# Kernel tuning notes

Hardware: AMD Instinct MI355X
Metric: run time of the kernel (lower is better)

## Reference

```python
import jax, jax.numpy as jnp
import numpy as np

NDIM = 128
GDIM = 128
NUM_LAYERS = 2
B = 8192
IDX = 16          # nodes per graph
EPG = 32          # edges per graph
N = B * IDX       # total nodes = 131072
E = B * EPG       # total edges = 262144


def setup_inputs() -> dict:
    key = jax.random.key(0)
    ks = jax.random.split(key, 24)
    h = jax.random.normal(ks[0], (B, IDX, NDIM), dtype=jnp.float32)
    # edges constrained within each graph (flattened node indexing)
    gid = jnp.repeat(jnp.arange(B, dtype=jnp.int64), EPG)
    src = gid * IDX + jax.random.randint(ks[1], (E,), 0, IDX).astype(jnp.int64)
    dst = gid * IDX + jax.random.randint(ks[2], (E,), 0, IDX).astype(jnp.int64)
    edge_index = jnp.stack([src, dst], axis=0)
    s = 0.05
    inp = {
        'h': h,
        'edge_index': edge_index,
        'msg_W': jax.random.normal(ks[3], (NUM_LAYERS, 2 * NDIM, 2 * NDIM), jnp.float32) * s,
        'msg_b': jax.random.normal(ks[4], (NUM_LAYERS, 2 * NDIM), jnp.float32) * s,
        'msgr_W': jax.random.normal(ks[5], (NUM_LAYERS, 2 * NDIM, 2 * NDIM), jnp.float32) * s,
        'msgr_b': jax.random.normal(ks[6], (NUM_LAYERS, 2 * NDIM), jnp.float32) * s,
        'gru_Wih': jax.random.normal(ks[7], (NUM_LAYERS, 3 * NDIM, 2 * NDIM), jnp.float32) * s,
        'gru_Whh': jax.random.normal(ks[8], (NUM_LAYERS, 3 * NDIM, NDIM), jnp.float32) * s,
        'gru_bih': jax.random.normal(ks[9], (NUM_LAYERS, 3 * NDIM), jnp.float32) * s,
        'gru_bhh': jax.random.normal(ks[10], (NUM_LAYERS, 3 * NDIM), jnp.float32) * s,
        'fm_W': jax.random.normal(ks[11], (GDIM, NDIM), jnp.float32) * s,
        'fm_b': jax.random.normal(ks[12], (GDIM,), jnp.float32) * s,
        'gm_W': jax.random.normal(ks[13], (1, NDIM), jnp.float32) * s,
        'gm_b': jax.random.normal(ks[14], (1,), jnp.float32) * s,
        'fmi_W': jax.random.normal(ks[15], (GDIM, NDIM), jnp.float32) * s,
        'fmi_b': jax.random.normal(ks[16], (GDIM,), jnp.float32) * s,
        'gmi_W': jax.random.normal(ks[17], (1, NDIM), jnp.float32) * s,
        'gmi_b': jax.random.normal(ks[18], (1,), jnp.float32) * s,
    }
    return inp


def _gnn_forward(h, edge_index, msg_W, msg_b, msgr_W, msgr_b,
                 gru_Wih, gru_Whh, gru_bih, gru_bhh):
    # h: [N, ndim]; edge_index: [2, E] -> doubled with reversed edges -> [2, 2E]
    ei = jnp.concatenate([edge_index, edge_index[::-1]], axis=1)
    src, dst = ei[0], ei[1]
    e = edge_index.shape[1]
    n_nodes = h.shape[0]
    for l in range(NUM_LAYERS):
        # (eval mode: dropout p=0.0 is a no-op)
        h_j = h[src]                       # [2E, ndim]
        h_i = h[dst]                       # [2E, ndim]
        m = jnp.concatenate([h_j, h_i], axis=1)   # [2E, 2*ndim]
        m_fwd, m_rev = m[:e], m[e:]
        a = jnp.concatenate([
            m_fwd @ msg_W[l].T + msg_b[l],
            m_rev @ msgr_W[l].T + msgr_b[l],
        ], axis=0)                          # [2E, 2*ndim]
        aggr = jax.ops.segment_sum(a, dst, num_segments=n_nodes)  # [N, 2*ndim]
        # GRUCell(aggr, h): gate order r, z, n (torch convention)
        gi = aggr @ gru_Wih[l].T + gru_bih[l]   # [N, 3*ndim]
        gh = h @ gru_Whh[l].T + gru_bhh[l]      # [N, 3*ndim]
        gi_r, gi_z, gi_n = jnp.split(gi, 3, axis=1)
        gh_r, gh_z, gh_n = jnp.split(gh, 3, axis=1)
        r = jax.nn.sigmoid(gi_r + gh_r)
        z = jax.nn.sigmoid(gi_z + gh_z)
        n = jnp.tanh(gi_n + r * gh_n)
        h = n + z * (h - n)                 # (1-z)*n + z*h
    return h


def _graph_aggr(h, idx, f_W, f_b, g_W, g_b):
    # gated sum aggregation
    h_vG = h @ f_W.T + f_b                      # [N, gdim]
    g_vG = jax.nn.sigmoid(h @ g_W.T + g_b)      # [N, 1]
    out = (h_vG * g_vG).reshape(-1, idx, f_W.shape[0])
    return out.sum(axis=1)                      # [B, gdim]


def reference(h, edge_index, msg_W, msg_b, msgr_W, msgr_b,
              gru_Wih, gru_Whh, gru_bih, gru_bhh,
              fm_W, fm_b, gm_W, gm_b, fmi_W, fmi_b, gmi_W, gmi_b):
    idx = h.shape[1]
    hf = h.reshape(-1, NDIM)
    hf = _gnn_forward(hf, edge_index, msg_W, msg_b, msgr_W, msgr_b,
                      gru_Wih, gru_Whh, gru_bih, gru_bhh)
    h_G = _graph_aggr(hf, idx, fm_W, fm_b, gm_W, gm_b)
    h_G_init = _graph_aggr(hf, idx, fmi_W, fmi_b, gmi_W, gmi_b)
    return (hf.reshape(-1, idx, NDIM), h_G, h_G_init)
```

## Files before the change

### kernel.cpp

```cpp
#include <hip/hip_runtime.h>
#include <math.h>
#include <stdint.h>

#define NDIM 128
#define B_GRAPHS 8192
#define IDX 16
#define EPG 32
#define NN (B_GRAPHS*IDX)
#define NE (B_GRAPHS*EPG)

typedef short bf16x8 __attribute__((ext_vector_type(8)));
typedef float f32x4  __attribute__((ext_vector_type(4)));

__device__ inline unsigned short f2bf(float x) {
    union { float f; unsigned u; } v; v.f = x;
    unsigned r = v.u + 0x7fff + ((v.u >> 16) & 1);
    return (unsigned short)(r >> 16);
}
__device__ inline float bf2f(unsigned short b) {
    union { unsigned u; float f; } v; v.u = ((unsigned)b) << 16;
    return v.f;
}
__device__ inline float sigm(float x) { return 1.f/(1.f + __expf(-x)); }
__device__ inline float tanh_f(float x) {
    float ax = fabsf(x);
    float t  = __expf(-2.f*ax);
    float r  = (1.f - t)/(1.f + t);
    return copysignf(r, x);
}

#define GLOAD_LDS16(g, l) \
    __builtin_amdgcn_global_load_lds( \
        (const __attribute__((address_space(1))) unsigned int*)(g), \
        (__attribute__((address_space(3))) unsigned int*)(l), 16, 0, 0)

__global__ __launch_bounds__(256) void compose_kernel(
    const float* __restrict__ msg_W, const float* __restrict__ msgr_W,
    const float* __restrict__ Wih,   const float* __restrict__ Whh,
    const float* __restrict__ msg_b, const float* __restrict__ msgr_b,
    unsigned short* __restrict__ WB, float* __restrict__ c34)
{
    int idx = blockIdx.x*256 + threadIdx.x;
    const int TWB = 2*512*640;
    if (idx < TWB) {
        int l = idx / (512*640); int rem = idx - l*(512*640);
        int cold = rem / 640; int k = rem - cold*640;
        float val;
        if (k < 512) {
            if (cold < 384) {
                const float* wih = Wih + l*384*256 + cold*256;
                const float* M; int sc;
                if (k < 128)      { M = msg_W  + l*256*256; sc = k;       }
                else if (k < 256) { M = msgr_W + l*256*256; sc = k - 128; }
                else if (k < 384) { M = msg_W  + l*256*256; sc = k - 128; }
                else              { M = msgr_W + l*256*256; sc = k - 256; }
                float acc = 0.f;
                for (int q = 0; q < 256; q++) acc = fmaf(wih[q], M[q*256 + sc], acc);
                val = acc;
            } else val = 0.f;
        } else {
            int kk = k - 512;
            if (cold < 256)      val = Whh[l*384*128 + cold*128 + kk];
            else if (cold < 384) val = 0.f;
            else                 val = Whh[l*384*128 + (cold-128)*128 + kk];
        }
        int cc = cold & 127, t = cold >> 7;
        int colp = ((cc >> 4) << 6) + (t << 4) + (cc & 15);
        WB[l*512*640 + colp*640 + k] = f2bf(val);
    } else if (idx < TWB + 2*2*384) {
        int i2 = idx - TWB;
        int l = i2 / 768; int rem = i2 - l*768;
        int which = rem / 384; int r = rem - which*384;
        const float* wih = Wih + l*384*256 + r*256;
        const float* bb  = (which ? msgr_b : msg_b) + l*256;
        float acc = 0.f;
        for (int q = 0; q < 256; q++) acc = fmaf(wih[q], bb[q], acc);
        c34[l*768 + which*384 + r] = acc;
    }
}

__global__ __launch_bounds__(128) void init_kernel(
    const float* __restrict__ hin, const int* __restrict__ ei,
    unsigned short* __restrict__ A, float* __restrict__ indeg,
    float* __restrict__ outdeg, unsigned char* __restrict__ pack)
{
    int g = blockIdx.x, t = threadIdx.x;
    __shared__ float hb[16][128];
    __shared__ float sin_[16][128];
    __shared__ float sout_[16][128];
    __shared__ int sl[32], dl[32];
    __shared__ int cin[16], cout[16];
    __shared__ int flag64;
    int base = g*IDX;
    for (int r = 0; r < 16; r++) hb[r][t] = hin[(size_t)(base+r)*128 + t];
    for (int r = 0; r < 16; r++) { sin_[r][t] = 0.f; sout_[r][t] = 0.f; }
    if (t < 16) { cin[t] = 0; cout[t] = 0; }
    if (t == 0) {
        int orv = 0;
        for (int i = 1; i < 64; i += 2) orv |= ei[i];
        flag64 = (orv == 0);
    }
    __syncthreads();
    if (t < 32) {
        int e = g*EPG + t;
        int sv, dv;
        if (flag64) { sv = ei[2*e]; dv = ei[2*(NE + e)]; }
        else        { sv = ei[e];   dv = ei[NE + e];     }
        sl[t] = sv - base; dl[t] = dv - base;
        atomicAdd(&cout[sl[t]], 1); atomicAdd(&cin[dl[t]], 1);
        pack[g*32 + t] = (unsigned char)((sl[t] & 15) | ((dl[t] & 15) << 4));
    }
    __syncthreads();
    for (int e = 0; e < 32; e++) {
        sin_[dl[e]][t]  += hb[sl[e]][t];
        sout_[sl[e]][t] += hb[dl[e]][t];
    }
    for (int r = 0; r < 16; r++) {
        size_t v = base + r;
        float di = (float)cin[r], dof = (float)cout[r];
        A[v*640 + t]        = f2bf(sin_[r][t]);
        A[v*640 + 128 + t]  = f2bf(sout_[r][t]);
        A[v*640 + 256 + t]  = f2bf(di  * hb[r][t]);
        A[v*640 + 384 + t]  = f2bf(dof * hb[r][t]);
        A[v*640 + 512 + t]  = f2bf(hb[r][t]);
    }
    if (t < 16) { indeg[base+t] = (float)cin[t]; outdeg[base+t] = (float)cout[t]; }
}

struct FSmem {
    unsigned short As[3][128*32];
    union {
        unsigned short Bs[3][384*32];
        unsigned short hnewB[128*128];
    } u;
    unsigned char csr[8][2][17];
    unsigned char adj[8][2][32];
    unsigned char offj[8][2][16];
    float gates[2][128];
};

__device__ __forceinline__ int h_addr(int row, int c) {
    return row*256 + (((c>>3) ^ (row&7))<<4) + ((c&7)<<1);
}

#define MF(a,b,c) __builtin_amdgcn_mfma_f32_16x16x32_bf16((a),(b),(c),0,0,0)

#define CSTEP(BUF, J2) do {                                                   \
    const unsigned short* Asb = sm.As[BUF];                                   \
    const unsigned short* Bsb = sm.u.Bs[BUF];                                 \
    bf16x8 bfv[3];                                                            \
    _Pragma("unroll")                                                         \
    for (int t = 0; t < 3; t++) {                                             \
        int a0 = wid*48 + t*16 + l15;                                         \
        bfv[t] = *(const bf16x8*)(Bsb + a0*32 + (l4 ^ ((a0>>2)&3))*8);        \
    }                                                                         \
    _Pragma("unroll")                                                         \
    for (int mi = 0; mi < 8; mi++) {                                          \
        int row = mi*16 + l15;                                                \
        bf16x8 af = *(const bf16x8*)(Asb + row*32 + (l4 ^ ((row>>2)&3))*8);   \
        acc[mi][0]  = MF(af, bfv[0], acc[mi][0]);                             \
        acc[mi][1]  = MF(af, bfv[1], acc[mi][1]);                             \
        acc[mi][J2] = MF(af, bfv[2], acc[mi][J2]);                            \
    }                                                                         \
} while (0)

template <bool FINAL>
__global__ __launch_bounds__(512, 2) void fused_kernel(
    unsigned short* __restrict__ A,
    const unsigned short* __restrict__ WBl,
    const float* __restrict__ indeg, const float* __restrict__ outdeg,
    const unsigned char* __restrict__ pack,
    const float* __restrict__ c34l,
    const float* __restrict__ bihl, const float* __restrict__ bhhl,
    const float* __restrict__ gmW,  const float* __restrict__ gmb,
    const float* __restrict__ gmiW, const float* __restrict__ gmib,
    float* __restrict__ hf, float* __restrict__ P1, float* __restrict__ P2,
    float* __restrict__ sg)
{
    __shared__ FSmem sm;
    const int n0  = blockIdx.x * 128;
    const int g0  = blockIdx.x * 8;
    const int tid = threadIdx.x;
    const int lane = tid & 63, wid = tid >> 6;
    const int l15 = lane & 15, l4 = lane >> 4;

    const int arow = tid >> 2, as_ = tid & 3;
    const int asrc = (as_ ^ ((arow >> 2) & 3)) * 8;
    const int adst = tid * 8;
    int bcol0[3], bcol1[3], bsrc[3], bdst[3];
#pragma unroll
    for (int i = 0; i < 3; i++) {
        int u = i*512 + tid;
        int a = u >> 2, s = u & 3;
        int grp = a / 48, rem = a - grp*48;
        int t = rem >> 4, clo = rem & 15;
        bcol0[i] = grp*64 + t*16 + clo;
        bcol1[i] = grp*64 + ((t==2) ? 48 : t*16) + clo;
        bsrc[i] = (s ^ ((a >> 2) & 3)) * 8;
        bdst[i] = u * 8;
    }

    auto STAGE = [&](int kst) {
        int b = kst % 3;
        GLOAD_LDS16(A + (size_t)(n0 + arow)*640 + kst*32 + asrc, sm.As[b] + adst);
        const unsigned short* WBk = WBl + kst*32;
        bool p1 = kst < 16;
#pragma unroll
        for (int i = 0; i < 3; i++) {
            int cp = p1 ? bcol0[i] : bcol1[i];
            GLOAD_LDS16(WBk + (size_t)cp*640 + bsrc[i], sm.u.Bs[b] + bdst[i]);
        }
    };

    f32x4 acc[8][4] = {};

    STAGE(0); STAGE(1);
    asm volatile("s_waitcnt vmcnt(4)\n\ts_barrier" ::: "memory");
    for (int ks = 0; ks < 16; ks++) {
        STAGE(ks + 2);
        CSTEP(ks % 3, 2);
        asm volatile("s_waitcnt vmcnt(4)\n\ts_barrier" ::: "memory");
    }
    for (int ks = 16; ks < 20; ks++) {
        if (ks < 18) STAGE(ks + 2);
        CSTEP(ks % 3, 3);
        if (ks < 18)
            asm volatile("s_waitcnt vmcnt(4)\n\ts_barrier" ::: "memory");
        else if (ks == 18)
            asm volatile("s_waitcnt vmcnt(0)\n\ts_barrier" ::: "memory");
    }
    __syncthreads();

    {
        const int chn = wid*16 + l15;
        float c3r = c34l[chn],     c3z = c34l[128+chn], c3n = c34l[256+chn];
        float c4r = c34l[384+chn], c4z = c34l[512+chn], c4n = c34l[640+chn];
        float br   = bihl[chn]     + bhhl[chn];
        float bz   = bihl[128+chn] + bhhl[128+chn];
        float bin_ = bihl[256+chn];
        float bhn_ = bhhl[256+chn];
#pragma unroll
        for (int mi = 0; mi < 8; mi++) {
#pragma unroll
            for (int q = 0; q < 4; q++) {
                int row = mi*16 + l4*4 + q;
                size_t v = (size_t)n0 + row;
                float di = indeg[v], dof = outdeg[v];
                float hold = bf2f(A[v*640 + 512 + chn]);
                float rr = sigm(acc[mi][0][q] + di*c3r + dof*c4r + br);
                float zz = sigm(acc[mi][1][q] + di*c3z + dof*c4z + bz);
                float nn = tanh_f(acc[mi][2][q] + di*c3n + dof*c4n + bin_
                                  + rr*(acc[mi][3][q] + bhn_));
                float hv = nn + zz*(hold - nn);
                *(unsigned short*)((char*)sm.u.hnewB + h_addr(row, chn)) = f2bf(hv);
                if (FINAL) hf[v*128 + chn] = hv;
            }
        }
    }
    __syncthreads();

    if (!FINAL) {
        if (tid < 16) {
            int gl = tid >> 1, dir = tid & 1;
            const unsigned char* pk = pack + (size_t)(g0 + gl)*32;
            unsigned char* C = sm.csr[gl][dir];
            for (int d = 0; d < 17; d++) C[d] = 0;
            for (int e = 0; e < 32; e++) {
                int p = pk[e];
                int key = dir ? (p & 15) : (p >> 4);
                C[key + 1]++;
            }
            for (int d = 0; d < 16; d++) { C[d+1] += C[d]; sm.offj[gl][dir][d] = C[d]; }
            for (int e = 0; e < 32; e++) {
                int p = pk[e];
                int key = dir ? (p & 15) : (p >> 4);
                int val = dir ? (p >> 4) : (p & 15);
                sm.adj[gl][dir][sm.offj[gl][dir][key]++] = val;
            }
        }
        __syncthreads();
        int c = tid & 127, gq = tid >> 7;
#pragma unroll
        for (int gi2 = 0; gi2 < 2; gi2++) {
            int gl = gq + gi2*4, rb = gl*16;
            for (int d = 0; d < 16; d++) {
                float a = 0.f;
                int e0 = sm.csr[gl][0][d], e1 = sm.csr[gl][0][d+1];
                for (int j = e0; j < e1; j++)
                    a += bf2f(*(const unsigned short*)((const char*)sm.u.hnewB
                            + h_addr(rb + sm.adj[gl][0][j], c)));
                float b = 0.f;
                int f0 = sm.csr[gl][1][d], f1 = sm.csr[gl][1][d+1];
                for (int j = f0; j < f1; j++)
                    b += bf2f(*(const unsigned short*)((const char*)sm.u.hnewB
                            + h_addr(rb + sm.adj[gl][1][j], c)));
                int row = rb + d;
                size_t v = (size_t)n0 + row;
                float hv = bf2f(*(const unsigned short*)((const char*)sm.u.hnewB
                            + h_addr(row, c)));
                float di  = (float)(e1 - e0);
                float dof = (float)(f1 - f0);
                A[v*640 + c]       = f2bf(a);
                A[v*640 + 128 + c] = f2bf(b);
                A[v*640 + 256 + c] = f2bf(di  * hv);
                A[v*640 + 384 + c] = f2bf(dof * hv);
                A[v*640 + 512 + c] = f2bf(hv);
            }
        }
    } else {
        if (tid < 128) {
            int row = tid;
            float a1 = 0.f, a2 = 0.f;
            for (int s = 0; s < 16; s++) {
                bf16x8 hv8 = *(const bf16x8*)((const char*)sm.u.hnewB
                              + row*256 + ((s ^ (row & 7)) << 4));
#pragma unroll
                for (int j = 0; j < 8; j++) {
                    float x = bf2f((unsigned short)hv8[j]);
                    int c = s*8 + j;
                    a1 = fmaf(gmW[c],  x, a1);
                    a2 = fmaf(gmiW[c], x, a2);
                }
            }
            sm.gates[0][row] = sigm(a1 + gmb[0]);
            sm.gates[1][row] = sigm(a2 + gmib[0]);
        }
        __syncthreads();
        int c = tid & 127, gq = tid >> 7;
#pragma unroll
        for (int gi2 = 0; gi2 < 2; gi2++) {
            int gl = gq + gi2*4, rb = gl*16;
            float p1 = 0.f, p2 = 0.f;
            for (int r = 0; r < 16; r++) {
                float x = bf2f(*(const unsigned short*)((const char*)sm.u.hnewB
                               + h_addr(rb + r, c)));
                p1 = fmaf(sm.gates[0][rb + r], x, p1);
                p2 = fmaf(sm.gates[1][rb + r], x, p2);
            }
            size_t g = g0 + gl;
            P1[g*128 + c] = p1;
            P2[g*128 + c] = p2;
        }
        if (tid < 16) {
            int gl = tid >> 1, w = tid & 1;
            float s = 0.f;
            for (int r = 0; r < 16; r++) s += sm.gates[w][gl*16 + r];
            sg[(size_t)(g0 + gl)*2 + w] = s;
        }
    }
}

__global__ __launch_bounds__(256) void outgemm_kernel(
    const float* __restrict__ P1, const float* __restrict__ P2,
    const float* __restrict__ sg,
    const float* __restrict__ fm_W,  const float* __restrict__ fm_b,
    const float* __restrict__ fmi_W, const float* __restrict__ fmi_b,
    float* __restrict__ out1, float* __restrict__ out2)
{
    const int g0 = blockIdx.x * 32;
    const int t  = threadIdx.x;
    __shared__ float Ws[128][33];
    __shared__ float Ps[32][33];
    const int tc = t & 15, tg = t >> 4;

    for (int pass = 0; pass < 2; pass++) {
        const float* P  = pass ? P2 : P1;
        const float* W  = pass ? fmi_W : fm_W;
        const float* bb = pass ? fmi_b : fm_b;
        float acc[2][8] = {};
        for (int kc = 0; kc < 128; kc += 32) {
#pragma unroll
            for (int i = 0; i < 16; i++) {
                int u = i*256 + t; int r = u >> 5, k = u & 31;
                Ws[r][k] = W[(size_t)r*128 + kc + k];
            }
#pragma unroll
            for (int i = 0; i < 4; i++) {
                int u = i*256 + t; int r = u >> 5, k = u & 31;
                Ps[r][k] = P[(size_t)(g0 + r)*128 + kc + k];
            }
            __syncthreads();
#pragma unroll 8
            for (int k = 0; k < 32; k++) {
                float p0 = Ps[tg*2][k], p1v = Ps[tg*2+1][k];
#pragma unroll
                for (int j = 0; j < 8; j++) {
                    float w = Ws[tc*8+j][k];
                    acc[0][j] = fmaf(p0,  w, acc[0][j]);
                    acc[1][j] = fmaf(p1v, w, acc[1][j]);
                }
            }
            __syncthreads();
        }
        float* outp = pass ? out2 : out1;
#pragma unroll
        for (int i = 0; i < 2; i++) {
            int g = g0 + tg*2 + i;
            float sgv = sg[g*2 + pass];
#pragma unroll
            for (int j = 0; j < 8; j++) {
                int cc = tc*8 + j;
                outp[(size_t)g*128 + cc] = acc[i][j] + bb[cc]*sgv;
            }
        }
    }
}

extern "C" void kernel_launch(void* const* d_in, const int* in_sizes, int n_in,
                              void* d_out, int out_size, void* d_ws, size_t ws_size,
                              hipStream_t stream)
{
    const float* h     = (const float*)d_in[0];
    const int*   ei    = (const int*)d_in[1];
    const float* msgW  = (const float*)d_in[2];
    const float* msgb  = (const float*)d_in[3];
    const float* msgrW = (const float*)d_in[4];
    const float* msgrb = (const float*)d_in[5];
    const float* Wih   = (const float*)d_in[6];
    const float* Whh   = (const float*)d_in[7];
    const float* bih   = (const float*)d_in[8];
    const float* bhh   = (const float*)d_in[9];
    const float* fmW   = (const float*)d_in[10];
    const float* fmb   = (const float*)d_in[11];
    const float* gmW   = (const float*)d_in[12];
    const float* gmb   = (const float*)d_in[13];
    const float* fmiW  = (const float*)d_in[14];
    const float* fmib  = (const float*)d_in[15];
    const float* gmiW  = (const float*)d_in[16];
    const float* gmib  = (const float*)d_in[17];

    char* w = (char*)d_ws;
    unsigned short* A    = (unsigned short*)w;  w += (size_t)NN*640*2;
    unsigned short* WB   = (unsigned short*)w;  w += (size_t)2*512*640*2;
    float* c34   = (float*)w;                   w += (size_t)2*768*4;
    float* indeg = (float*)w;                   w += (size_t)NN*4;
    float* outdeg= (float*)w;                   w += (size_t)NN*4;
    unsigned char* pack = (unsigned char*)w;    w += (size_t)B_GRAPHS*32;
    float* P1    = (float*)w;                   w += (size_t)B_GRAPHS*128*4;
    float* P2    = (float*)w;                   w += (size_t)B_GRAPHS*128*4;
    float* sgb   = (float*)w;                   w += (size_t)B_GRAPHS*2*4;

    float* hf   = (float*)d_out;
    float* out1 = hf + (size_t)NN*128;
    float* out2 = out1 + (size_t)B_GRAPHS*128;

    int compose_items = 2*512*640 + 2*2*384;
    compose_kernel<<<(compose_items + 255)/256, 256, 0, stream>>>(
        msgW, msgrW, Wih, Whh, msgb, msgrb, WB, c34);

    init_kernel<<<B_GRAPHS, 128, 0, stream>>>(h, ei, A, indeg, outdeg, pack);

    fused_kernel<false><<<NN/128, 512, 0, stream>>>(
        A, WB, indeg, outdeg, pack, c34, bih, bhh,
        gmW, gmb, gmiW, gmib, nullptr, nullptr, nullptr, nullptr);
    fused_kernel<true><<<NN/128, 512, 0, stream>>>(
        A, WB + (size_t)512*640, indeg, outdeg, pack,
        c34 + 768, bih + 384, bhh + 384,
        gmW, gmb, gmiW, gmib, hf, P1, P2, sgb);

    outgemm_kernel<<<B_GRAPHS/32, 256, 0, stream>>>(
        P1, P2, sgb, fmW, fmb, fmiW, fmib, out1, out2);
}
```

Before: 438.9 us.

## Halve fused kernel row tile to 64 and switch to double-buffered staging

Shrinks the fused GEMM+GRU kernel's node tile from 128 to 64 rows (4 graphs per block), doubling the grid, and replaces the 3-stage LDS pipeline with a 2-stage one that waits for all loads at every step. Only half the waves load A rows. The per-graph CSR/adjacency build is hoisted ahead of the GEMM main loop so it is no longer serialized after the epilogue. The aim is more blocks and less LDS per block for better occupancy. The cost is that each 384-column weight tile is reloaded twice as often, and the deeper prefetch overlap is lost.

```diff
diff --git a/kernel.cpp b/kernel.cpp
--- a/kernel.cpp
+++ b/kernel.cpp
@@ -128,18 +128,18 @@
 }
 
 struct FSmem {
-    unsigned short As[3][128*32];
+    unsigned short As[2][64*32];
     union {
-        unsigned short Bs[3][384*32];
-        unsigned short hnewB[128*128];
+        unsigned short Bs[2][384*32];
+        unsigned short hnewB[64*128];
     } u;
-    unsigned char csr[8][2][17];
-    unsigned char adj[8][2][32];
-    unsigned char offj[8][2][16];
-    float gates[2][128];
+    unsigned char csr[4][2][17];
+    unsigned char adj[4][2][32];
+    unsigned char offj[4][2][16];
+    float gates[2][64];
 };
 
-__device__ __forceinline__ int h_addr(int row, int c) {
+__device__ __forceinline__ int hn_addr(int row, int c) {
     return row*256 + (((c>>3) ^ (row&7))<<4) + ((c&7)<<1);
 }
 
@@ -150,12 +150,12 @@
     const unsigned short* Bsb = sm.u.Bs[BUF];                                 \
     bf16x8 bfv[3];                                                            \
     _Pragma("unroll")                                                         \
-    for (int t = 0; t < 3; t++) {                                             \
-        int a0 = wid*48 + t*16 + l15;                                         \
-        bfv[t] = *(const bf16x8*)(Bsb + a0*32 + (l4 ^ ((a0>>2)&3))*8);        \
+    for (int tt = 0; tt < 3; tt++) {                                          \
+        int a0 = wid*48 + tt*16 + l15;                                        \
+        bfv[tt] = *(const bf16x8*)(Bsb + a0*32 + (l4 ^ ((a0>>2)&3))*8);       \
     }                                                                         \
     _Pragma("unroll")                                                         \
-    for (int mi = 0; mi < 8; mi++) {                                          \
+    for (int mi = 0; mi < 4; mi++) {                                          \
         int row = mi*16 + l15;                                                \
         bf16x8 af = *(const bf16x8*)(Asb + row*32 + (l4 ^ ((row>>2)&3))*8);   \
         acc[mi][0]  = MF(af, bfv[0], acc[mi][0]);                             \
@@ -178,31 +178,55 @@
     float* __restrict__ sg)
 {
     __shared__ FSmem sm;
-    const int n0  = blockIdx.x * 128;
-    const int g0  = blockIdx.x * 8;
+    const int n0  = blockIdx.x * 64;
+    const int g0  = blockIdx.x * 4;
     const int tid = threadIdx.x;
     const int lane = tid & 63, wid = tid >> 6;
     const int l15 = lane & 15, l4 = lane >> 4;
 
-    const int arow = tid >> 2, as_ = tid & 3;
+    const int u0   = wid*64 + lane;
+    const int arow = u0 >> 2, as_ = u0 & 3;
     const int asrc = (as_ ^ ((arow >> 2) & 3)) * 8;
-    const int adst = tid * 8;
+    const int adst = u0 * 8;
     int bcol0[3], bcol1[3], bsrc[3], bdst[3];
 #pragma unroll
     for (int i = 0; i < 3; i++) {
         int u = i*512 + tid;
         int a = u >> 2, s = u & 3;
         int grp = a / 48, rem = a - grp*48;
-        int t = rem >> 4, clo = rem & 15;
-        bcol0[i] = grp*64 + t*16 + clo;
-        bcol1[i] = grp*64 + ((t==2) ? 48 : t*16) + clo;
+        int tt = rem >> 4, clo = rem & 15;
+        bcol0[i] = grp*64 + tt*16 + clo;
+        bcol1[i] = grp*64 + ((tt==2) ? 48 : tt*16) + clo;
         bsrc[i] = (s ^ ((a >> 2) & 3)) * 8;
         bdst[i] = u * 8;
     }
 
+    if (!FINAL) {
+        if (tid < 8) {
+            int gl = tid >> 1, dir = tid & 1;
+            const unsigned char* pk = pack + (size_t)(g0 + gl)*32;
+            unsigned char* C = sm.csr[gl][dir];
+            for (int d = 0; d < 17; d++) C[d] = 0;
+            for (int e = 0; e < 32; e++) {
+                int p = pk[e];
+                int key = dir ? (p & 15) : (p >> 4);
+                C[key + 1]++;
+            }
+            for (int d = 0; d < 16; d++) { C[d+1] += C[d]; sm.offj[gl][dir][d] = C[d]; }
+            for (int e = 0; e < 32; e++) {
+                int p = pk[e];
+                int key = dir ? (p & 15) : (p >> 4);
+                int val = dir ? (p >> 4) : (p & 15);
+                sm.adj[gl][dir][sm.offj[gl][dir][key]++] = val;
+            }
+        }
+    }
+
     auto STAGE = [&](int kst) {
-        int b = kst % 3;
-        GLOAD_LDS16(A + (size_t)(n0 + arow)*640 + kst*32 + asrc, sm.As[b] + adst);
+        int b = kst & 1;
+        if (wid < 4)
+            GLOAD_LDS16(A + (size_t)(n0 + arow)*640 + kst*32 + asrc,
+                        sm.As[b] + adst);
         const unsigned short* WBk = WBl + kst*32;
         bool p1 = kst < 16;
 #pragma unroll
@@ -212,24 +236,16 @@
         }
     };
 
-    f32x4 acc[8][4] = {};
-
-    STAGE(0); STAGE(1);
-    asm volatile("s_waitcnt vmcnt(4)\n\ts_barrier" ::: "memory");
-    for (int ks = 0; ks < 16; ks++) {
-        STAGE(ks + 2);
-        CSTEP(ks % 3, 2);
-        asm volatile("s_waitcnt vmcnt(4)\n\ts_barrier" ::: "memory");
-    }
-    for (int ks = 16; ks < 20; ks++) {
-        if (ks < 18) STAGE(ks + 2);
-        CSTEP(ks % 3, 3);
-        if (ks < 18)
-            asm volatile("s_waitcnt vmcnt(4)\n\ts_barrier" ::: "memory");
-        else if (ks == 18)
-            asm volatile("s_waitcnt vmcnt(0)\n\ts_barrier" ::: "memory");
-    }
-    __syncthreads();
+    f32x4 acc[4][4] = {};
+
+    STAGE(0);
+    asm volatile("s_waitcnt vmcnt(0)\n\ts_barrier" ::: "memory");
+    for (int ks = 0; ks < 20; ks++) {
+        if (ks + 1 < 20) STAGE(ks + 1);
+        if (ks < 16) CSTEP(ks & 1, 2);
+        else         CSTEP(ks & 1, 3);
+        asm volatile("s_waitcnt vmcnt(0)\n\ts_barrier" ::: "memory");
+    }
 
     {
         const int chn = wid*16 + l15;
@@ -240,7 +256,7 @@
         float bin_ = bihl[256+chn];
         float bhn_ = bhhl[256+chn];
 #pragma unroll
-        for (int mi = 0; mi < 8; mi++) {
+        for (int mi = 0; mi < 4; mi++) {
 #pragma unroll
             for (int q = 0; q < 4; q++) {
                 int row = mi*16 + l4*4 + q;
@@ -252,63 +268,42 @@
                 float nn = tanh_f(acc[mi][2][q] + di*c3n + dof*c4n + bin_
                                   + rr*(acc[mi][3][q] + bhn_));
                 float hv = nn + zz*(hold - nn);
-                *(unsigned short*)((char*)sm.u.hnewB + h_addr(row, chn)) = f2bf(hv);
                 if (FINAL) hf[v*128 + chn] = hv;
+                *(unsigned short*)((char*)sm.u.hnewB + hn_addr(row, chn))
+                    = f2bf(hv);
             }
         }
     }
     __syncthreads();
 
     if (!FINAL) {
-        if (tid < 16) {
-            int gl = tid >> 1, dir = tid & 1;
-            const unsigned char* pk = pack + (size_t)(g0 + gl)*32;
-            unsigned char* C = sm.csr[gl][dir];
-            for (int d = 0; d < 17; d++) C[d] = 0;
-            for (int e = 0; e < 32; e++) {
-                int p = pk[e];
-                int key = dir ? (p & 15) : (p >> 4);
-                C[key + 1]++;
-            }
-            for (int d = 0; d < 16; d++) { C[d+1] += C[d]; sm.offj[gl][dir][d] = C[d]; }
-            for (int e = 0; e < 32; e++) {
-                int p = pk[e];
-                int key = dir ? (p & 15) : (p >> 4);
-                int val = dir ? (p >> 4) : (p & 15);
-                sm.adj[gl][dir][sm.offj[gl][dir][key]++] = val;
-            }
-        }
-        __syncthreads();
-        int c = tid & 127, gq = tid >> 7;
-#pragma unroll
-        for (int gi2 = 0; gi2 < 2; gi2++) {
-            int gl = gq + gi2*4, rb = gl*16;
-            for (int d = 0; d < 16; d++) {
-                float a = 0.f;
-                int e0 = sm.csr[gl][0][d], e1 = sm.csr[gl][0][d+1];
-                for (int j = e0; j < e1; j++)
-                    a += bf2f(*(const unsigned short*)((const char*)sm.u.hnewB
-                            + h_addr(rb + sm.adj[gl][0][j], c)));
-                float b = 0.f;
-                int f0 = sm.csr[gl][1][d], f1 = sm.csr[gl][1][d+1];
-                for (int j = f0; j < f1; j++)
-                    b += bf2f(*(const unsigned short*)((const char*)sm.u.hnewB
-                            + h_addr(rb + sm.adj[gl][1][j], c)));
-                int row = rb + d;
-                size_t v = (size_t)n0 + row;
-                float hv = bf2f(*(const unsigned short*)((const char*)sm.u.hnewB
-                            + h_addr(row, c)));
-                float di  = (float)(e1 - e0);
-                float dof = (float)(f1 - f0);
-                A[v*640 + c]       = f2bf(a);
-                A[v*640 + 128 + c] = f2bf(b);
-                A[v*640 + 256 + c] = f2bf(di  * hv);
-                A[v*640 + 384 + c] = f2bf(dof * hv);
-                A[v*640 + 512 + c] = f2bf(hv);
-            }
+        int c = tid & 127, gl = tid >> 7;
+        int rb = gl*16;
+        for (int d = 0; d < 16; d++) {
+            float a = 0.f;
+            int e0 = sm.csr[gl][0][d], e1 = sm.csr[gl][0][d+1];
+            for (int j = e0; j < e1; j++)
+                a += bf2f(*(const unsigned short*)((const char*)sm.u.hnewB
+                        + hn_addr(rb + sm.adj[gl][0][j], c)));
+            float b = 0.f;
+            int f0 = sm.csr[gl][1][d], f1 = sm.csr[gl][1][d+1];
+            for (int j = f0; j < f1; j++)
+                b += bf2f(*(const unsigned short*)((const char*)sm.u.hnewB
+                        + hn_addr(rb + sm.adj[gl][1][j], c)));
+            int row = rb + d;
+            size_t v = (size_t)n0 + row;
+            float hv = bf2f(*(const unsigned short*)((const char*)sm.u.hnewB
+                        + hn_addr(row, c)));
+            float di  = (float)(e1 - e0);
+            float dof = (float)(f1 - f0);
+            A[v*640 + c]       = f2bf(a);
+            A[v*640 + 128 + c] = f2bf(b);
+            A[v*640 + 256 + c] = f2bf(di  * hv);
+            A[v*640 + 384 + c] = f2bf(dof * hv);
+            A[v*640 + 512 + c] = f2bf(hv);
         }
     } else {
-        if (tid < 128) {
+        if (tid < 64) {
             int row = tid;
             float a1 = 0.f, a2 = 0.f;
             for (int s = 0; s < 16; s++) {
@@ -327,21 +322,18 @@
         }
         __syncthreads();
         int c = tid & 127, gq = tid >> 7;
-#pragma unroll
-        for (int gi2 = 0; gi2 < 2; gi2++) {
-            int gl = gq + gi2*4, rb = gl*16;
-            float p1 = 0.f, p2 = 0.f;
-            for (int r = 0; r < 16; r++) {
-                float x = bf2f(*(const unsigned short*)((const char*)sm.u.hnewB
-                               + h_addr(rb + r, c)));
-                p1 = fmaf(sm.gates[0][rb + r], x, p1);
-                p2 = fmaf(sm.gates[1][rb + r], x, p2);
-            }
-            size_t g = g0 + gl;
-            P1[g*128 + c] = p1;
-            P2[g*128 + c] = p2;
-        }
-        if (tid < 16) {
+        int rb = gq*16;
+        float p1 = 0.f, p2 = 0.f;
+        for (int r = 0; r < 16; r++) {
+            float x = bf2f(*(const unsigned short*)((const char*)sm.u.hnewB
+                           + hn_addr(rb + r, c)));
+            p1 = fmaf(sm.gates[0][rb + r], x, p1);
+            p2 = fmaf(sm.gates[1][rb + r], x, p2);
+        }
+        size_t g = g0 + gq;
+        P1[g*128 + c] = p1;
+        P2[g*128 + c] = p2;
+        if (tid < 8) {
             int gl = tid >> 1, w = tid & 1;
             float s = 0.f;
             for (int r = 0; r < 16; r++) s += sm.gates[w][gl*16 + r];
@@ -450,10 +442,10 @@
 
     init_kernel<<<B_GRAPHS, 128, 0, stream>>>(h, ei, A, indeg, outdeg, pack);
 
-    fused_kernel<false><<<NN/128, 512, 0, stream>>>(
+    fused_kernel<false><<<NN/64, 512, 0, stream>>>(
         A, WB, indeg, outdeg, pack, c34, bih, bhh,
         gmW, gmb, gmiW, gmib, nullptr, nullptr, nullptr, nullptr);
-    fused_kernel<true><<<NN/128, 512, 0, stream>>>(
+    fused_kernel<true><<<NN/64, 512, 0, stream>>>(
         A, WB + (size_t)512*640, indeg, outdeg, pack,
         c34 + 768, bih + 384, bhh + 384,
         gmW, gmb, gmiW, gmib, hf, P1, P2, sgb);
```

New measurement: 540.2 us. +23.1%, slower.
